# Performance work log

Measured on AMD Instinct MI355X. Metric: run time of the kernel, lower is better.

## Reference

```python
import jax, jax.numpy as jnp
import numpy as np
import math

B, T, C, H, RANK, RD = 8, 512, 2048, 16, 8, 16
HD = C // H  # 128
ADAPTER_SCALE = 1.0 / RANK  # scale / rank with scale=1.0


def setup_inputs() -> dict:
    key = jax.random.key(0)
    ks = jax.random.split(key, 7)
    x = jax.random.normal(ks[0], (B, T, C), dtype=jnp.float32)
    # frozen random linears (weights ~ N(0,1)/sqrt(in_features))
    Wqkv = jax.random.normal(ks[1], (3 * C, C), dtype=jnp.float32) / math.sqrt(C)
    Wout = jax.random.normal(ks[2], (C, C), dtype=jnp.float32) / math.sqrt(C)
    # VeRA frozen random matrices
    A0_qkv = jax.random.normal(ks[3], (RANK, C), dtype=jnp.float32) / math.sqrt(C)
    B0_qkv = jax.random.normal(ks[4], (3 * C, RANK), dtype=jnp.float32) / math.sqrt(RANK)
    A0_out = jax.random.normal(ks[5], (RANK, C), dtype=jnp.float32) / math.sqrt(C)
    B0_out = jax.random.normal(ks[6], (C, RANK), dtype=jnp.float32) / math.sqrt(RANK)
    # learned scaling vectors (init to ones, as in the module)
    d_a_qkv = jnp.ones((RANK,), dtype=jnp.float32)
    d_b_qkv = jnp.ones((RANK,), dtype=jnp.float32)
    d_a_out = jnp.ones((RANK,), dtype=jnp.float32)
    d_b_out = jnp.ones((RANK,), dtype=jnp.float32)
    # partial RoPE caches over first RD dims
    freqs = 1.0 / (10000.0 ** (jnp.arange(0, RD, 2, dtype=jnp.float32) / RD))  # [RD/2]
    ang = jnp.arange(T, dtype=jnp.float32)[:, None] * freqs[None, :]  # [T, RD/2]
    cos = jnp.cos(ang)
    sin = jnp.sin(ang)
    return {"x": x, "Wqkv": Wqkv, "A0_qkv": A0_qkv, "B0_qkv": B0_qkv,
            "d_a_qkv": d_a_qkv, "d_b_qkv": d_b_qkv,
            "Wout": Wout, "A0_out": A0_out, "B0_out": B0_out,
            "d_a_out": d_a_out, "d_b_out": d_b_out,
            "cos": cos, "sin": sin}


def _adapted_linear(x, W, A0, B0, d_a, d_b):
    # frozen(x) + VeRA adapter: diag(d_b) B0 diag(d_a) A0, scaled by 1/rank
    base = x @ W.T
    h = (x @ A0.T) * (d_a * d_b)
    return base + (h @ B0.T) * ADAPTER_SCALE


def _apply_rope(q, cos, sin):
    # q: [B, H, T, HD]; rotate first RD dims, pass-through the rest
    x_rope, x_pass = q[..., :RD], q[..., RD:]
    half = RD // 2
    x1, x2 = x_rope[..., :half], x_rope[..., half:]
    c = cos[None, None]  # [1,1,T,RD/2]
    s = sin[None, None]
    rot = jnp.concatenate([x1 * c - x2 * s, x2 * c + x1 * s], axis=-1)
    return jnp.concatenate([rot, x_pass], axis=-1)


def reference(x, Wqkv, A0_qkv, B0_qkv, d_a_qkv, d_b_qkv,
              Wout, A0_out, B0_out, d_a_out, d_b_out, cos, sin):
    qkv = _adapted_linear(x, Wqkv, A0_qkv, B0_qkv, d_a_qkv, d_b_qkv)  # [B,T,3C]
    qkv = qkv.reshape(B, T, 3, H, HD)
    q = jnp.transpose(qkv[:, :, 0], (0, 2, 1, 3))  # [B,H,T,HD]
    k = jnp.transpose(qkv[:, :, 1], (0, 2, 1, 3))
    v = jnp.transpose(qkv[:, :, 2], (0, 2, 1, 3))
    q = _apply_rope(q, cos, sin)
    k = _apply_rope(k, cos, sin)
    # causal SDPA
    scale = 1.0 / math.sqrt(HD)
    scores = jnp.einsum('bhqd,bhkd->bhqk', q, k) * scale
    mask = jnp.tril(jnp.ones((T, T), dtype=bool))
    scores = jnp.where(mask[None, None], scores, jnp.finfo(scores.dtype).min)
    attn = jax.nn.softmax(scores, axis=-1)
    y = jnp.einsum('bhqk,bhkd->bhqd', attn, v)  # [B,H,T,HD]
    y = jnp.transpose(y, (0, 2, 1, 3)).reshape(B, T, C)
    return _adapted_linear(y, Wout, A0_out, B0_out, d_a_out, d_b_out)
```

## Files before the change

kernel.cpp:

```cpp
#include <hip/hip_runtime.h>

typedef unsigned short ushort_t;
typedef __attribute__((ext_vector_type(8))) short short8;
typedef __attribute__((ext_vector_type(4))) float f32x4;

#define AS1(p) ((const __attribute__((address_space(1))) void*)(p))
#define AS3(p) ((__attribute__((address_space(3))) void*)(p))

__device__ __forceinline__ ushort_t f2bf(float f){
  unsigned u = __float_as_uint(f);
  u += 0x7FFFu + ((u>>16)&1u);
  return (ushort_t)(u>>16);
}
__device__ __forceinline__ float bf2f(ushort_t h){
  return __uint_as_float(((unsigned)h)<<16);
}

__global__ __launch_bounds__(256) void conv_f2b(const float* __restrict__ src,
                                                ushort_t* __restrict__ dst, int n){
  int i = (blockIdx.x*256 + threadIdx.x)*4;
  if (i < n){
    float4 v = *(const float4*)&src[i];
    ushort_t o0=f2bf(v.x), o1=f2bf(v.y), o2=f2bf(v.z), o3=f2bf(v.w);
    ushort4 o; o.x=o0; o.y=o1; o.z=o2; o.w=o3;
    *(ushort4*)&dst[i] = o;
  }
}

template<bool BF16IN>
__global__ __launch_bounds__(256) void lora_h(const void* __restrict__ X,
                                              const float* __restrict__ A0,
                                              const float* __restrict__ da,
                                              const float* __restrict__ db,
                                              float* __restrict__ out, int K){
  int m = blockIdx.x;
  int tid = threadIdx.x, lane = tid & 63, w = tid >> 6;
  float part[8] = {0,0,0,0,0,0,0,0};
  for (int k = tid; k < K; k += 256){
    float xv;
    if (BF16IN) xv = bf2f(((const ushort_t*)X)[(size_t)m*K + k]);
    else        xv = ((const float*)X)[(size_t)m*K + k];
    #pragma unroll
    for (int r=0;r<8;++r) part[r] += xv * A0[r*K + k];
  }
  #pragma unroll
  for (int r=0;r<8;++r)
    for (int d=1;d<64;d<<=1) part[r] += __shfl_xor(part[r], d, 64);
  __shared__ float wsum[4][8];
  if (lane==0){
    #pragma unroll
    for (int r=0;r<8;++r) wsum[w][r] = part[r];
  }
  __syncthreads();
  if (tid < 8){
    float s = wsum[0][tid]+wsum[1][tid]+wsum[2][tid]+wsum[3][tid];
    out[(size_t)m*8 + tid] = s * da[tid]*db[tid];
  }
}

template<int MODE>
__global__ __launch_bounds__(512, 1) void gemm128x256_lora(
    const ushort_t* __restrict__ A, const ushort_t* __restrict__ Bw,
    const float* __restrict__ hmat, const float* __restrict__ B0,
    void* __restrict__ C, int M, int N, int K)
{
  __shared__ __align__(16) char smem[98304];
  const int tid = threadIdx.x, lane = tid & 63, w = tid >> 6;
  const int wm = w >> 2, wn = w & 3;

  const int nbn = N >> 8;
  const int nwg = (M >> 7) * nbn;
  const int q8 = nwg >> 3;
  const int swz = ((int)blockIdx.x & 7)*q8 + ((int)blockIdx.x >> 3);
  const int m0 = (swz / nbn) << 7, n0 = (swz % nbn) << 8;

  const int NTt = K >> 6;

  const int srow8  = tid >> 3;
  const int schunk = (lane & 7) ^ (lane >> 3);

  #define STAGE_AU(u, tt, bb) do { \
    const ushort_t* g_ = A + (size_t)(m0 + (u)*64 + srow8)*K + (tt)*64 + schunk*8; \
    __builtin_amdgcn_global_load_lds(AS1(g_), AS3(smem + (bb)*16384 + (u)*8192 + w*1024), 16, 0, 0); \
  } while(0)
  #define STAGE_BU(u, tt, bb) do { \
    const ushort_t* g_ = Bw + (size_t)(n0 + (u)*64 + srow8)*K + (tt)*64 + schunk*8; \
    __builtin_amdgcn_global_load_lds(AS1(g_), AS3(smem + 32768 + (bb)*32768 + (u)*8192 + w*1024), 16, 0, 0); \
  } while(0)

  #define RDA(bb, q, kk) (*(const short8*)(smem + (bb)*16384 + \
      ((q)*32 + wm*16 + (lane&15))*128 + ((((kk)*4 + (lane>>4)) ^ (lane&7))<<4)))
  #define RDB(bb, rg, kk) (*(const short8*)(smem + 32768 + (bb)*32768 + \
      ((rg)*64 + wn*16 + (lane&15))*128 + ((((kk)*4 + (lane>>4)) ^ (lane&7))<<4)))

  #define MM0(q,rl) do{ \
    acc[q][rl] = __builtin_amdgcn_mfma_f32_16x16x32_bf16(aF[q][0], bF[rl][0], acc[q][rl], 0,0,0); \
    acc[q][rl] = __builtin_amdgcn_mfma_f32_16x16x32_bf16(aF[q][1], bF[rl][1], acc[q][rl], 0,0,0); \
  }while(0)
  #define MM1(q,rl) do{ \
    acc[q][(rl)+2] = __builtin_amdgcn_mfma_f32_16x16x32_bf16(aF[q][0], bF[rl][0], acc[q][(rl)+2], 0,0,0); \
    acc[q][(rl)+2] = __builtin_amdgcn_mfma_f32_16x16x32_bf16(aF[q][1], bF[rl][1], acc[q][(rl)+2], 0,0,0); \
  }while(0)

  #define BARRIER() asm volatile("s_barrier" ::: "memory")

  short8 aF[4][2];
  short8 bF[2][2];
  f32x4 acc[4][4] = {};

  STAGE_AU(0,0,0); STAGE_AU(1,0,0); STAGE_BU(0,0,0); STAGE_BU(1,0,0);
  STAGE_BU(2,0,0); STAGE_BU(3,0,0);
  asm volatile("s_waitcnt vmcnt(2)" ::: "memory");
  BARRIER();

  for (int t = 0; t < NTt-1; ++t){
    const int b = t & 1, nb = b ^ 1;
    #pragma unroll
    for (int q=0;q<4;++q){ aF[q][0]=RDA(b,q,0); aF[q][1]=RDA(b,q,1); }
    #pragma unroll
    for (int rl=0;rl<2;++rl){ bF[rl][0]=RDB(b,rl,0); bF[rl][1]=RDB(b,rl,1); }
    STAGE_AU(0,t+1,nb); STAGE_AU(1,t+1,nb); STAGE_BU(0,t+1,nb); STAGE_BU(1,t+1,nb);
    __builtin_amdgcn_s_setprio(1);
    MM0(0,0); MM0(0,1); MM0(1,0); MM0(1,1);
    MM0(2,0); MM0(2,1); MM0(3,0); MM0(3,1);
    __builtin_amdgcn_s_setprio(0);
    asm volatile("s_waitcnt vmcnt(4)" ::: "memory");
    BARRIER();
    #pragma unroll
    for (int rl=0;rl<2;++rl){ bF[rl][0]=RDB(b,rl+2,0); bF[rl][1]=RDB(b,rl+2,1); }
    STAGE_BU(2,t+1,nb); STAGE_BU(3,t+1,nb);
    __builtin_amdgcn_s_setprio(1);
    MM1(0,0); MM1(0,1); MM1(1,0); MM1(1,1);
    MM1(2,0); MM1(2,1); MM1(3,0); MM1(3,1);
    __builtin_amdgcn_s_setprio(0);
    asm volatile("s_waitcnt lgkmcnt(0)" ::: "memory");
    asm volatile("s_waitcnt vmcnt(2)" ::: "memory");
    BARRIER();
  }

  {
    const int b = (NTt-1) & 1;
    #pragma unroll
    for (int q=0;q<4;++q){ aF[q][0]=RDA(b,q,0); aF[q][1]=RDA(b,q,1); }
    #pragma unroll
    for (int rl=0;rl<2;++rl){ bF[rl][0]=RDB(b,rl,0); bF[rl][1]=RDB(b,rl,1); }
    __builtin_amdgcn_s_setprio(1);
    MM0(0,0); MM0(0,1); MM0(1,0); MM0(1,1);
    MM0(2,0); MM0(2,1); MM0(3,0); MM0(3,1);
    __builtin_amdgcn_s_setprio(0);
    asm volatile("s_waitcnt vmcnt(0)" ::: "memory");
    BARRIER();
    #pragma unroll
    for (int rl=0;rl<2;++rl){ bF[rl][0]=RDB(b,rl+2,0); bF[rl][1]=RDB(b,rl+2,1); }
    MM1(0,0); MM1(0,1); MM1(1,0); MM1(1,1);
    MM1(2,0); MM1(2,1); MM1(3,0); MM1(3,1);
  }

  float b0v[4][8];
  #pragma unroll
  for (int r=0;r<4;++r){
    int col = n0 + r*64 + wn*16 + (lane&15);
    const float4* bp = (const float4*)&B0[(size_t)col*8];
    float4 u0 = bp[0], u1 = bp[1];
    b0v[r][0]=u0.x; b0v[r][1]=u0.y; b0v[r][2]=u0.z; b0v[r][3]=u0.w;
    b0v[r][4]=u1.x; b0v[r][5]=u1.y; b0v[r][6]=u1.z; b0v[r][7]=u1.w;
  }
  #pragma unroll
  for (int q=0;q<4;++q){
    #pragma unroll
    for (int jj=0;jj<4;++jj){
      int row = m0 + q*32 + wm*16 + (lane>>4)*4 + jj;
      const float4* hp = (const float4*)&hmat[(size_t)row*8];
      float4 h0 = hp[0], h1 = hp[1];
      #pragma unroll
      for (int r=0;r<4;++r){
        float lor = h0.x*b0v[r][0]+h0.y*b0v[r][1]+h0.z*b0v[r][2]+h0.w*b0v[r][3]
                  + h1.x*b0v[r][4]+h1.y*b0v[r][5]+h1.z*b0v[r][6]+h1.w*b0v[r][7];
        int col = n0 + r*64 + wn*16 + (lane&15);
        float v = acc[q][r][jj] + 0.125f*lor;
        if (MODE==0) ((ushort_t*)C)[(size_t)row*N + col] = f2bf(v);
        else         ((float*)C)[(size_t)row*N + col]    = v;
      }
    }
  }
  #undef STAGE_AU
  #undef STAGE_BU
  #undef RDA
  #undef RDB
  #undef MM0
  #undef MM1
  #undef BARRIER
}

__global__ __launch_bounds__(256) void rope_kernel(ushort_t* __restrict__ qkv,
                                                   const float* __restrict__ cosb,
                                                   const float* __restrict__ sinb){
  int idx = blockIdx.x*256 + threadIdx.x;
  int d = idx & 7;
  int g = idx >> 3;
  int h_ = g & 15;
  int s  = (g>>4) & 1;
  int t  = (g>>5) & 511;
  int b  = g >> 14;
  size_t base = (size_t)(b*512 + t)*6144 + s*2048 + h_*128;
  float x1 = bf2f(qkv[base+d]), x2 = bf2f(qkv[base+d+8]);
  float c = cosb[t*8+d], sn = sinb[t*8+d];
  qkv[base+d]   = f2bf(x1*c - x2*sn);
  qkv[base+d+8] = f2bf(x2*c + x1*sn);
}

__global__ __launch_bounds__(256) void attn_kernel(const ushort_t* __restrict__ qkv,
                                                   ushort_t* __restrict__ y){
  __shared__ __align__(16) ushort_t Ks[64*128];
  __shared__ __align__(16) ushort_t Vt[128*64];
  __shared__ __align__(16) ushort_t Pl[4][16*64];

  const int qt = blockIdx.x, hh = blockIdx.y, b = blockIdx.z;
  const int tid = threadIdx.x, lane = tid & 63, w = tid >> 6, g = lane >> 4;
  const int qb0 = qt*64;
  const int row_base = b*512;
  const int qoff = hh*128;
  const int koff = 2048 + hh*128;
  const int voff = 4096 + hh*128;
  const float scale = 0.08838834764831845f;

  short8 qf[4];
  {
    int qr = qb0 + w*16 + (lane & 15);
    const ushort_t* qp = qkv + (size_t)(row_base + qr)*6144 + qoff + g*8;
    #pragma unroll
    for (int kc=0;kc<4;++kc) qf[kc] = *(const short8*)(qp + kc*32);
  }

  const int krow = tid >> 4;
  const int kc_  = tid & 15;
  const int kcs  = (kc_ & 8) | ((kc_ ^ (krow & 7)) & 7);
  const int vr   = tid >> 2;
  const int vd0  = (tid & 3) * 32;
  const int vrhi = vr >> 3, vrlo = vr & 7;

  f32x4 o[8] = {};
  float mrow[4] = {-1e30f,-1e30f,-1e30f,-1e30f};
  float lrow[4] = {0,0,0,0};

  for (int t = 0; t <= qt; ++t){
    const int kv0 = t*64;
    __syncthreads();
    {
      const ushort_t* kg = qkv + (size_t)(row_base + kv0 + krow)*6144 + koff + kcs*8;
      #pragma unroll
      for (int i=0;i<4;++i)
        __builtin_amdgcn_global_load_lds(AS1(kg + (size_t)(i*16)*6144),
                                         AS3((char*)Ks + i*4096 + tid*16), 16, 0, 0);
    }
    {
      const ushort_t* vg = qkv + (size_t)(row_base + kv0 + vr)*6144 + voff + vd0;
      short8 vv0 = ((const short8*)vg)[0];
      short8 vv1 = ((const short8*)vg)[1];
      short8 vv2 = ((const short8*)vg)[2];
      short8 vv3 = ((const short8*)vg)[3];
      #pragma unroll
      for (int ii=0;ii<8;++ii){
        int sw = (vrhi ^ ii) << 3;
        Vt[(vd0 + ii     )*64 + sw + vrlo] = (ushort_t)vv0[ii];
        Vt[(vd0 + 8 + ii )*64 + sw + vrlo] = (ushort_t)vv1[ii];
        Vt[(vd0 + 16 + ii)*64 + sw + vrlo] = (ushort_t)vv2[ii];
        Vt[(vd0 + 24 + ii)*64 + sw + vrlo] = (ushort_t)vv3[ii];
      }
    }
    __syncthreads();

    f32x4 s4[4] = {};
    #pragma unroll
    for (int cg=0;cg<4;++cg){
      const int row = cg*16 + (lane&15);
      const int rx = row & 7;
      #pragma unroll
      for (int kc=0;kc<4;++kc){
        const int ch = kc*4 + g;
        const short8 kfv = *(const short8*)&Ks[row*128 + (((ch&8)|((ch^rx)&7))<<3)];
        s4[cg] = __builtin_amdgcn_mfma_f32_16x16x32_bf16(qf[kc], kfv, s4[cg], 0, 0, 0);
      }
    }

    const bool diag = (t == qt);
    float fac[4], p0[4], p1[4], p2[4], p3[4];
    #pragma unroll
    for (int j=0;j<4;++j){
      float a0 = s4[0][j]*scale, a1 = s4[1][j]*scale, a2 = s4[2][j]*scale, a3 = s4[3][j]*scale;
      if (diag){
        int q_abs = qb0 + w*16 + g*4 + j;
        int c0 = kv0 + (lane&15);
        if (c0      > q_abs) a0 = -1e30f;
        if (c0 + 16 > q_abs) a1 = -1e30f;
        if (c0 + 32 > q_abs) a2 = -1e30f;
        if (c0 + 48 > q_abs) a3 = -1e30f;
      }
      float mx = fmaxf(fmaxf(a0,a1), fmaxf(a2,a3));
      #pragma unroll
      for (int d=1; d<16; d<<=1) mx = fmaxf(mx, __shfl_xor(mx, d, 16));
      float mn = fmaxf(mrow[j], mx);
      float f  = __expf(mrow[j] - mn);
      mrow[j] = mn; fac[j] = f;
      p0[j] = __expf(a0 - mn); p1[j] = __expf(a1 - mn);
      p2[j] = __expf(a2 - mn); p3[j] = __expf(a3 - mn);
      float rs = p0[j] + p1[j] + p2[j] + p3[j];
      #pragma unroll
      for (int d=1; d<16; d<<=1) rs += __shfl_xor(rs, d, 16);
      lrow[j] = lrow[j]*f + rs;
    }
    #pragma unroll
    for (int n=0;n<8;++n){
      #pragma unroll
      for (int j=0;j<4;++j) o[n][j] *= fac[j];
    }

    {
      ushort_t* plw = &Pl[w][0];
      #pragma unroll
      for (int j=0;j<4;++j){
        const int prow = g*4 + j;
        const int rx = prow & 7;
        const int cl = (lane&15)>>3, c7 = lane&7;
        plw[prow*64 + (((0*2+cl)^rx)<<3) + c7] = f2bf(p0[j]);
        plw[prow*64 + (((1*2+cl)^rx)<<3) + c7] = f2bf(p1[j]);
        plw[prow*64 + (((2*2+cl)^rx)<<3) + c7] = f2bf(p2[j]);
        plw[prow*64 + (((3*2+cl)^rx)<<3) + c7] = f2bf(p3[j]);
      }
    }
    {
      const ushort_t* plw = &Pl[w][0];
      const int rowP = lane & 15, rxp = rowP & 7;
      const short8 pf0 = *(const short8*)&plw[rowP*64 + (((g  )^rxp)<<3)];
      const short8 pf1 = *(const short8*)&plw[rowP*64 + (((4+g)^rxp)<<3)];
      #pragma unroll
      for (int n=0;n<8;++n){
        const int d = n*16 + (lane&15);
        const int dx = d & 7;
        const short8 vf0 = *(const short8*)&Vt[d*64 + (((g  )^dx)<<3)];
        const short8 vf1 = *(const short8*)&Vt[d*64 + (((4+g)^dx)<<3)];
        o[n] = __builtin_amdgcn_mfma_f32_16x16x32_bf16(pf0, vf0, o[n], 0, 0, 0);
        o[n] = __builtin_amdgcn_mfma_f32_16x16x32_bf16(pf1, vf1, o[n], 0, 0, 0);
      }
    }
  }

  #pragma unroll
  for (int j=0;j<4;++j){
    float inv = 1.0f / lrow[j];
    int qr = qb0 + w*16 + g*4 + j;
    #pragma unroll
    for (int n=0;n<8;++n)
      y[(size_t)(row_base+qr)*2048 + hh*128 + n*16 + (lane&15)] = f2bf(o[n][j]*inv);
  }
}

extern "C" void kernel_launch(void* const* d_in, const int* in_sizes, int n_in,
                              void* d_out, int out_size, void* d_ws, size_t ws_size,
                              hipStream_t stream){
  const float* x       = (const float*)d_in[0];
  const float* Wqkv    = (const float*)d_in[1];
  const float* A0_qkv  = (const float*)d_in[2];
  const float* B0_qkv  = (const float*)d_in[3];
  const float* da_qkv  = (const float*)d_in[4];
  const float* db_qkv  = (const float*)d_in[5];
  const float* Wout    = (const float*)d_in[6];
  const float* A0_out  = (const float*)d_in[7];
  const float* B0_out  = (const float*)d_in[8];
  const float* da_out  = (const float*)d_in[9];
  const float* db_out  = (const float*)d_in[10];
  const float* cosb    = (const float*)d_in[11];
  const float* sinb    = (const float*)d_in[12];
  float* out = (float*)d_out;

  char* ws = (char*)d_ws;
  ushort_t* x_bf    = (ushort_t*)(ws);
  ushort_t* wqkv_bf = (ushort_t*)(ws + 16777216);
  ushort_t* wout_bf = (ushort_t*)(ws + 41943040);
  ushort_t* qkv_bf  = (ushort_t*)(ws + 50331648);
  ushort_t* y_bf    = (ushort_t*)(ws + 100663296);
  float*    h_qkv   = (float*)   (ws + 117440512);
  float*    h_out   = (float*)   (ws + 117571584);

  const int M = 4096;
  const int C = 2048;
  const int N3 = 6144;

  conv_f2b<<<8192, 256, 0, stream>>>(x,    x_bf,    M*C);
  conv_f2b<<<12288,256, 0, stream>>>(Wqkv, wqkv_bf, N3*C);
  conv_f2b<<<4096, 256, 0, stream>>>(Wout, wout_bf, C*C);

  lora_h<false><<<M, 256, 0, stream>>>(x, A0_qkv, da_qkv, db_qkv, h_qkv, C);

  gemm128x256_lora<0><<<(M/128)*(N3/256), 512, 0, stream>>>(x_bf, wqkv_bf, h_qkv, B0_qkv,
                                                            qkv_bf, M, N3, C);

  rope_kernel<<<4096, 256, 0, stream>>>(qkv_bf, cosb, sinb);

  attn_kernel<<<dim3(8, 16, 8), 256, 0, stream>>>(qkv_bf, y_bf);

  lora_h<true><<<M, 256, 0, stream>>>(y_bf, A0_out, da_out, db_out, h_out, C);

  gemm128x256_lora<1><<<(M/128)*(C/256), 512, 0, stream>>>(y_bf, wout_bf, h_out, B0_out,
                                                           out, M, C, C);
}
```

Measured before the change: 272.2 us.

## Use 256x256 tile GEMM for QKV projection and fuse x bf16 conversion into LoRA-h

Adds a new QKV GEMM kernel with a 256x256 output tile per workgroup, double-buffered LDS with interleaved half-tile staging and MFMA phases, and the VeRA adapter epilogue. The larger tile raises operand reuse and halves the number of workgroups. Separately, the fp32-to-bf16 conversion of x is folded into the LoRA h kernel, which already reads x, so the standalone conversion pass goes away. Risks: 96 workgroups on a large-CU device can underfill it, and the per-element ushort writes in the fused kernel are narrow.

```diff
diff --git a/kernel.cpp b/kernel.cpp
--- a/kernel.cpp
+++ b/kernel.cpp
@@ -27,19 +27,18 @@
   }
 }
 
-template<bool BF16IN>
-__global__ __launch_bounds__(256) void lora_h(const void* __restrict__ X,
-                                              const float* __restrict__ A0,
-                                              const float* __restrict__ da,
-                                              const float* __restrict__ db,
-                                              float* __restrict__ out, int K){
+__global__ __launch_bounds__(256) void lora_h_f32(const float* __restrict__ X,
+                                                  ushort_t* __restrict__ Xbf,
+                                                  const float* __restrict__ A0,
+                                                  const float* __restrict__ da,
+                                                  const float* __restrict__ db,
+                                                  float* __restrict__ out, int K){
   int m = blockIdx.x;
   int tid = threadIdx.x, lane = tid & 63, w = tid >> 6;
   float part[8] = {0,0,0,0,0,0,0,0};
   for (int k = tid; k < K; k += 256){
-    float xv;
-    if (BF16IN) xv = bf2f(((const ushort_t*)X)[(size_t)m*K + k]);
-    else        xv = ((const float*)X)[(size_t)m*K + k];
+    float xv = X[(size_t)m*K + k];
+    Xbf[(size_t)m*K + k] = f2bf(xv);
     #pragma unroll
     for (int r=0;r<8;++r) part[r] += xv * A0[r*K + k];
   }
@@ -56,6 +55,203 @@
     float s = wsum[0][tid]+wsum[1][tid]+wsum[2][tid]+wsum[3][tid];
     out[(size_t)m*8 + tid] = s * da[tid]*db[tid];
   }
+}
+
+__global__ __launch_bounds__(256) void lora_h_bf16(const ushort_t* __restrict__ X,
+                                                   const float* __restrict__ A0,
+                                                   const float* __restrict__ da,
+                                                   const float* __restrict__ db,
+                                                   float* __restrict__ out, int K){
+  int m = blockIdx.x;
+  int tid = threadIdx.x, lane = tid & 63, w = tid >> 6;
+  float part[8] = {0,0,0,0,0,0,0,0};
+  for (int k = tid; k < K; k += 256){
+    float xv = bf2f(X[(size_t)m*K + k]);
+    #pragma unroll
+    for (int r=0;r<8;++r) part[r] += xv * A0[r*K + k];
+  }
+  #pragma unroll
+  for (int r=0;r<8;++r)
+    for (int d=1;d<64;d<<=1) part[r] += __shfl_xor(part[r], d, 64);
+  __shared__ float wsum[4][8];
+  if (lane==0){
+    #pragma unroll
+    for (int r=0;r<8;++r) wsum[w][r] = part[r];
+  }
+  __syncthreads();
+  if (tid < 8){
+    float s = wsum[0][tid]+wsum[1][tid]+wsum[2][tid]+wsum[3][tid];
+    out[(size_t)m*8 + tid] = s * da[tid]*db[tid];
+  }
+}
+
+__global__ __launch_bounds__(512, 1) void gemm256_lora(
+    const ushort_t* __restrict__ A, const ushort_t* __restrict__ Bw,
+    const float* __restrict__ hmat, const float* __restrict__ B0,
+    ushort_t* __restrict__ C, int M, int N, int K)
+{
+  __shared__ __align__(16) char smem[131072];
+  const int tid = threadIdx.x, lane = tid & 63, w = tid >> 6;
+  const int wm = w >> 2, wn = w & 3;
+
+  const int nbn = N >> 8;
+  const int nwg = (M >> 8) * nbn;
+  const int q8 = nwg >> 3;
+  const int swz = ((int)blockIdx.x & 7)*q8 + ((int)blockIdx.x >> 3);
+  const int m0 = (swz / nbn) << 8, n0 = (swz % nbn) << 8;
+
+  const int NTt = K >> 6;
+  const int srow   = tid >> 3;
+  const int schunk = (lane & 7) ^ (lane >> 3);
+
+  #define STAGE_A(h, tt, bb) do { \
+    const ushort_t* g_ = A + (size_t)(m0 + (h)*128 + srow)*K + (tt)*64 + schunk*8; \
+    __builtin_amdgcn_global_load_lds(AS1(g_), AS3(smem + (bb)*32768 + (h)*16384 + tid*16), 16, 0, 0); \
+    __builtin_amdgcn_global_load_lds(AS1(g_ + (size_t)64*K), AS3(smem + (bb)*32768 + (h)*16384 + 8192 + tid*16), 16, 0, 0); \
+  } while(0)
+  #define STAGE_B(h, tt, bb) do { \
+    const ushort_t* g_ = Bw + (size_t)(n0 + (h)*128 + srow)*K + (tt)*64 + schunk*8; \
+    __builtin_amdgcn_global_load_lds(AS1(g_), AS3(smem + 65536 + (bb)*32768 + (h)*16384 + tid*16), 16, 0, 0); \
+    __builtin_amdgcn_global_load_lds(AS1(g_ + (size_t)64*K), AS3(smem + 65536 + (bb)*32768 + (h)*16384 + 8192 + tid*16), 16, 0, 0); \
+  } while(0)
+
+  #define RDA(bb, q, kk) (*(const short8*)(smem + (bb)*32768 + ((q)>>2)*16384 + \
+      (((q)&3)*32 + wm*16 + (lane&15))*128 + ((((kk)*4 + (lane>>4)) ^ (lane&7))<<4)))
+  #define RDB(bb, r, kk) (*(const short8*)(smem + 65536 + (bb)*32768 + ((r)>>1)*16384 + \
+      (((r)&1)*64 + wn*16 + (lane&15))*128 + ((((kk)*4 + (lane>>4)) ^ (lane&7))<<4)))
+
+  #define MM(q, ai, r, bi) do{ \
+    acc[q][r] = __builtin_amdgcn_mfma_f32_16x16x32_bf16(aF[ai][0], bF[bi][0], acc[q][r], 0,0,0); \
+    acc[q][r] = __builtin_amdgcn_mfma_f32_16x16x32_bf16(aF[ai][1], bF[bi][1], acc[q][r], 0,0,0); \
+  }while(0)
+
+  #define BARRIER() asm volatile("s_barrier" ::: "memory")
+  #define LGKM0()  do{ asm volatile("s_waitcnt lgkmcnt(0)" ::: "memory"); __builtin_amdgcn_sched_barrier(0); }while(0)
+
+  short8 aF[4][2];
+  short8 bF[2][2];
+  f32x4 acc[8][4] = {};
+
+  STAGE_A(0,0,0); STAGE_B(0,0,0); STAGE_A(1,0,0); STAGE_B(1,0,0);
+  asm volatile("s_waitcnt vmcnt(4)" ::: "memory");
+  BARRIER();
+
+  for (int t = 0; t < NTt-1; ++t){
+    const int b = t & 1, nb = b ^ 1;
+    #pragma unroll
+    for (int q=0;q<4;++q){ aF[q][0]=RDA(b,q,0); aF[q][1]=RDA(b,q,1); }
+    #pragma unroll
+    for (int rl=0;rl<2;++rl){ bF[rl][0]=RDB(b,rl,0); bF[rl][1]=RDB(b,rl,1); }
+    STAGE_A(0, t+1, nb);
+    BARRIER(); LGKM0();
+    __builtin_amdgcn_s_setprio(1);
+    MM(0,0,0,0); MM(0,0,1,1); MM(1,1,0,0); MM(1,1,1,1);
+    MM(2,2,0,0); MM(2,2,1,1); MM(3,3,0,0); MM(3,3,1,1);
+    __builtin_amdgcn_s_setprio(0);
+    asm volatile("s_waitcnt vmcnt(4)" ::: "memory");
+    BARRIER();
+    #pragma unroll
+    for (int q=0;q<4;++q){ aF[q][0]=RDA(b,q+4,0); aF[q][1]=RDA(b,q+4,1); }
+    STAGE_B(0, t+1, nb);
+    BARRIER(); LGKM0();
+    __builtin_amdgcn_s_setprio(1);
+    MM(4,0,0,0); MM(4,0,1,1); MM(5,1,0,0); MM(5,1,1,1);
+    MM(6,2,0,0); MM(6,2,1,1); MM(7,3,0,0); MM(7,3,1,1);
+    __builtin_amdgcn_s_setprio(0);
+    asm volatile("s_waitcnt vmcnt(4)" ::: "memory");
+    BARRIER();
+    #pragma unroll
+    for (int q=0;q<4;++q){ aF[q][0]=RDA(b,q,0); aF[q][1]=RDA(b,q,1); }
+    #pragma unroll
+    for (int rl=0;rl<2;++rl){ bF[rl][0]=RDB(b,rl+2,0); bF[rl][1]=RDB(b,rl+2,1); }
+    STAGE_A(1, t+1, nb);
+    BARRIER(); LGKM0();
+    __builtin_amdgcn_s_setprio(1);
+    MM(0,0,2,0); MM(0,0,3,1); MM(1,1,2,0); MM(1,1,3,1);
+    MM(2,2,2,0); MM(2,2,3,1); MM(3,3,2,0); MM(3,3,3,1);
+    __builtin_amdgcn_s_setprio(0);
+    BARRIER();
+    #pragma unroll
+    for (int q=0;q<4;++q){ aF[q][0]=RDA(b,q+4,0); aF[q][1]=RDA(b,q+4,1); }
+    STAGE_B(1, t+1, nb);
+    BARRIER(); LGKM0();
+    __builtin_amdgcn_s_setprio(1);
+    MM(4,0,2,0); MM(4,0,3,1); MM(5,1,2,0); MM(5,1,3,1);
+    MM(6,2,2,0); MM(6,2,3,1); MM(7,3,2,0); MM(7,3,3,1);
+    __builtin_amdgcn_s_setprio(0);
+    asm volatile("s_waitcnt vmcnt(4)" ::: "memory");
+    BARRIER();
+  }
+
+  {
+    const int b = (NTt-1) & 1;
+    #pragma unroll
+    for (int q=0;q<4;++q){ aF[q][0]=RDA(b,q,0); aF[q][1]=RDA(b,q,1); }
+    #pragma unroll
+    for (int rl=0;rl<2;++rl){ bF[rl][0]=RDB(b,rl,0); bF[rl][1]=RDB(b,rl,1); }
+    BARRIER(); LGKM0();
+    __builtin_amdgcn_s_setprio(1);
+    MM(0,0,0,0); MM(0,0,1,1); MM(1,1,0,0); MM(1,1,1,1);
+    MM(2,2,0,0); MM(2,2,1,1); MM(3,3,0,0); MM(3,3,1,1);
+    __builtin_amdgcn_s_setprio(0);
+    asm volatile("s_waitcnt vmcnt(2)" ::: "memory");
+    BARRIER();
+    #pragma unroll
+    for (int q=0;q<4;++q){ aF[q][0]=RDA(b,q+4,0); aF[q][1]=RDA(b,q+4,1); }
+    BARRIER(); LGKM0();
+    __builtin_amdgcn_s_setprio(1);
+    MM(4,0,0,0); MM(4,0,1,1); MM(5,1,0,0); MM(5,1,1,1);
+    MM(6,2,0,0); MM(6,2,1,1); MM(7,3,0,0); MM(7,3,1,1);
+    __builtin_amdgcn_s_setprio(0);
+    asm volatile("s_waitcnt vmcnt(0)" ::: "memory");
+    BARRIER();
+    #pragma unroll
+    for (int q=0;q<4;++q){ aF[q][0]=RDA(b,q,0); aF[q][1]=RDA(b,q,1); }
+    #pragma unroll
+    for (int rl=0;rl<2;++rl){ bF[rl][0]=RDB(b,rl+2,0); bF[rl][1]=RDB(b,rl+2,1); }
+    LGKM0();
+    MM(0,0,2,0); MM(0,0,3,1); MM(1,1,2,0); MM(1,1,3,1);
+    MM(2,2,2,0); MM(2,2,3,1); MM(3,3,2,0); MM(3,3,3,1);
+    BARRIER();
+    #pragma unroll
+    for (int q=0;q<4;++q){ aF[q][0]=RDA(b,q+4,0); aF[q][1]=RDA(b,q+4,1); }
+    LGKM0();
+    MM(4,0,2,0); MM(4,0,3,1); MM(5,1,2,0); MM(5,1,3,1);
+    MM(6,2,2,0); MM(6,2,3,1); MM(7,3,2,0); MM(7,3,3,1);
+  }
+
+  float b0v[4][8];
+  #pragma unroll
+  for (int r=0;r<4;++r){
+    int col = n0 + r*64 + wn*16 + (lane&15);
+    const float4* bp = (const float4*)&B0[(size_t)col*8];
+    float4 u0 = bp[0], u1 = bp[1];
+    b0v[r][0]=u0.x; b0v[r][1]=u0.y; b0v[r][2]=u0.z; b0v[r][3]=u0.w;
+    b0v[r][4]=u1.x; b0v[r][5]=u1.y; b0v[r][6]=u1.z; b0v[r][7]=u1.w;
+  }
+  #pragma unroll
+  for (int q=0;q<8;++q){
+    #pragma unroll
+    for (int jj=0;jj<4;++jj){
+      int row = m0 + q*32 + wm*16 + (lane>>4)*4 + jj;
+      const float4* hp = (const float4*)&hmat[(size_t)row*8];
+      float4 h0 = hp[0], h1 = hp[1];
+      #pragma unroll
+      for (int r=0;r<4;++r){
+        float lor = h0.x*b0v[r][0]+h0.y*b0v[r][1]+h0.z*b0v[r][2]+h0.w*b0v[r][3]
+                  + h1.x*b0v[r][4]+h1.y*b0v[r][5]+h1.z*b0v[r][6]+h1.w*b0v[r][7];
+        int col = n0 + r*64 + wn*16 + (lane&15);
+        C[(size_t)row*N + col] = f2bf(acc[q][r][jj] + 0.125f*lor);
+      }
+    }
+  }
+  #undef STAGE_A
+  #undef STAGE_B
+  #undef RDA
+  #undef RDB
+  #undef MM
+  #undef BARRIER
+  #undef LGKM0
 }
 
 template<int MODE>
@@ -386,20 +582,19 @@
   const int C = 2048;
   const int N3 = 6144;
 
-  conv_f2b<<<8192, 256, 0, stream>>>(x,    x_bf,    M*C);
   conv_f2b<<<12288,256, 0, stream>>>(Wqkv, wqkv_bf, N3*C);
   conv_f2b<<<4096, 256, 0, stream>>>(Wout, wout_bf, C*C);
 
-  lora_h<false><<<M, 256, 0, stream>>>(x, A0_qkv, da_qkv, db_qkv, h_qkv, C);
-
-  gemm128x256_lora<0><<<(M/128)*(N3/256), 512, 0, stream>>>(x_bf, wqkv_bf, h_qkv, B0_qkv,
-                                                            qkv_bf, M, N3, C);
+  lora_h_f32<<<M, 256, 0, stream>>>(x, x_bf, A0_qkv, da_qkv, db_qkv, h_qkv, C);
+
+  gemm256_lora<<<(M/256)*(N3/256), 512, 0, stream>>>(x_bf, wqkv_bf, h_qkv, B0_qkv,
+                                                     qkv_bf, M, N3, C);
 
   rope_kernel<<<4096, 256, 0, stream>>>(qkv_bf, cosb, sinb);
 
   attn_kernel<<<dim3(8, 16, 8), 256, 0, stream>>>(qkv_bf, y_bf);
 
-  lora_h<true><<<M, 256, 0, stream>>>(y_bf, A0_out, da_out, db_out, h_out, C);
+  lora_h_bf16<<<M, 256, 0, stream>>>(y_bf, A0_out, da_out, db_out, h_out, C);
 
   gemm128x256_lora<1><<<(M/128)*(C/256), 512, 0, stream>>>(y_bf, wout_bf, h_out, B0_out,
                                                            out, M, C, C);
```

Result: no change. 272.5 us (+0.1%).

## Triple-buffer GEMM K-tiles and fuse x bf16 conversion into LoRA down-projection

Applied to the files above, without the earlier changes.

The GEMM main loop moves from a double-buffered, half-tile interleaved schedule to a three-stage LDS ring. Each stage holds a full 128x256x64 tile, loads run two tiles ahead, and each iteration has one barrier. This is meant to hide global-load latency and cut barriers per K-step, at the cost of 144KB of LDS and more B-fragment registers. Separately, the fp32-to-bf16 conversion of x is folded into the lora_h kernel that already reads x, which removes one launch and one full read of x.

```diff
diff --git a/kernel.cpp b/kernel.cpp
--- a/kernel.cpp
+++ b/kernel.cpp
@@ -27,19 +27,46 @@
   }
 }
 
-template<bool BF16IN>
-__global__ __launch_bounds__(256) void lora_h(const void* __restrict__ X,
-                                              const float* __restrict__ A0,
-                                              const float* __restrict__ da,
-                                              const float* __restrict__ db,
-                                              float* __restrict__ out, int K){
+__global__ __launch_bounds__(256) void lora_h_f32(const float* __restrict__ X,
+                                                  ushort_t* __restrict__ Xbf,
+                                                  const float* __restrict__ A0,
+                                                  const float* __restrict__ da,
+                                                  const float* __restrict__ db,
+                                                  float* __restrict__ out, int K){
   int m = blockIdx.x;
   int tid = threadIdx.x, lane = tid & 63, w = tid >> 6;
   float part[8] = {0,0,0,0,0,0,0,0};
   for (int k = tid; k < K; k += 256){
-    float xv;
-    if (BF16IN) xv = bf2f(((const ushort_t*)X)[(size_t)m*K + k]);
-    else        xv = ((const float*)X)[(size_t)m*K + k];
+    float xv = X[(size_t)m*K + k];
+    Xbf[(size_t)m*K + k] = f2bf(xv);
+    #pragma unroll
+    for (int r=0;r<8;++r) part[r] += xv * A0[r*K + k];
+  }
+  #pragma unroll
+  for (int r=0;r<8;++r)
+    for (int d=1;d<64;d<<=1) part[r] += __shfl_xor(part[r], d, 64);
+  __shared__ float wsum[4][8];
+  if (lane==0){
+    #pragma unroll
+    for (int r=0;r<8;++r) wsum[w][r] = part[r];
+  }
+  __syncthreads();
+  if (tid < 8){
+    float s = wsum[0][tid]+wsum[1][tid]+wsum[2][tid]+wsum[3][tid];
+    out[(size_t)m*8 + tid] = s * da[tid]*db[tid];
+  }
+}
+
+__global__ __launch_bounds__(256) void lora_h_bf16(const ushort_t* __restrict__ X,
+                                                   const float* __restrict__ A0,
+                                                   const float* __restrict__ da,
+                                                   const float* __restrict__ db,
+                                                   float* __restrict__ out, int K){
+  int m = blockIdx.x;
+  int tid = threadIdx.x, lane = tid & 63, w = tid >> 6;
+  float part[8] = {0,0,0,0,0,0,0,0};
+  for (int k = tid; k < K; k += 256){
+    float xv = bf2f(X[(size_t)m*K + k]);
     #pragma unroll
     for (int r=0;r<8;++r) part[r] += xv * A0[r*K + k];
   }
@@ -64,7 +91,7 @@
     const float* __restrict__ hmat, const float* __restrict__ B0,
     void* __restrict__ C, int M, int N, int K)
 {
-  __shared__ __align__(16) char smem[98304];
+  __shared__ __align__(16) char smem[147456];
   const int tid = threadIdx.x, lane = tid & 63, w = tid >> 6;
   const int wm = w >> 2, wn = w & 3;
 
@@ -81,79 +108,82 @@
 
   #define STAGE_AU(u, tt, bb) do { \
     const ushort_t* g_ = A + (size_t)(m0 + (u)*64 + srow8)*K + (tt)*64 + schunk*8; \
-    __builtin_amdgcn_global_load_lds(AS1(g_), AS3(smem + (bb)*16384 + (u)*8192 + w*1024), 16, 0, 0); \
+    __builtin_amdgcn_global_load_lds(AS1(g_), AS3(smem + (bb)*49152 + (u)*8192 + w*1024), 16, 0, 0); \
   } while(0)
   #define STAGE_BU(u, tt, bb) do { \
     const ushort_t* g_ = Bw + (size_t)(n0 + (u)*64 + srow8)*K + (tt)*64 + schunk*8; \
-    __builtin_amdgcn_global_load_lds(AS1(g_), AS3(smem + 32768 + (bb)*32768 + (u)*8192 + w*1024), 16, 0, 0); \
+    __builtin_amdgcn_global_load_lds(AS1(g_), AS3(smem + (bb)*49152 + 16384 + (u)*8192 + w*1024), 16, 0, 0); \
   } while(0)
-
-  #define RDA(bb, q, kk) (*(const short8*)(smem + (bb)*16384 + \
+  #define STAGE_TILE(tt, bb) do { \
+    STAGE_AU(0,tt,bb); STAGE_AU(1,tt,bb); \
+    STAGE_BU(0,tt,bb); STAGE_BU(1,tt,bb); STAGE_BU(2,tt,bb); STAGE_BU(3,tt,bb); \
+  } while(0)
+
+  #define RDA(bb, q, kk) (*(const short8*)(smem + (bb)*49152 + \
       ((q)*32 + wm*16 + (lane&15))*128 + ((((kk)*4 + (lane>>4)) ^ (lane&7))<<4)))
-  #define RDB(bb, rg, kk) (*(const short8*)(smem + 32768 + (bb)*32768 + \
+  #define RDB(bb, rg, kk) (*(const short8*)(smem + (bb)*49152 + 16384 + \
       ((rg)*64 + wn*16 + (lane&15))*128 + ((((kk)*4 + (lane>>4)) ^ (lane&7))<<4)))
 
-  #define MM0(q,rl) do{ \
-    acc[q][rl] = __builtin_amdgcn_mfma_f32_16x16x32_bf16(aF[q][0], bF[rl][0], acc[q][rl], 0,0,0); \
-    acc[q][rl] = __builtin_amdgcn_mfma_f32_16x16x32_bf16(aF[q][1], bF[rl][1], acc[q][rl], 0,0,0); \
+  #define MM(q,r) do{ \
+    acc[q][r] = __builtin_amdgcn_mfma_f32_16x16x32_bf16(aF[q][0], bF[r][0], acc[q][r], 0,0,0); \
+    acc[q][r] = __builtin_amdgcn_mfma_f32_16x16x32_bf16(aF[q][1], bF[r][1], acc[q][r], 0,0,0); \
   }while(0)
-  #define MM1(q,rl) do{ \
-    acc[q][(rl)+2] = __builtin_amdgcn_mfma_f32_16x16x32_bf16(aF[q][0], bF[rl][0], acc[q][(rl)+2], 0,0,0); \
-    acc[q][(rl)+2] = __builtin_amdgcn_mfma_f32_16x16x32_bf16(aF[q][1], bF[rl][1], acc[q][(rl)+2], 0,0,0); \
-  }while(0)
 
   #define BARRIER() asm volatile("s_barrier" ::: "memory")
 
   short8 aF[4][2];
-  short8 bF[2][2];
+  short8 bF[4][2];
   f32x4 acc[4][4] = {};
 
-  STAGE_AU(0,0,0); STAGE_AU(1,0,0); STAGE_BU(0,0,0); STAGE_BU(1,0,0);
-  STAGE_BU(2,0,0); STAGE_BU(3,0,0);
-  asm volatile("s_waitcnt vmcnt(2)" ::: "memory");
+  STAGE_TILE(0, 0);
+  STAGE_TILE(1, 1);
+  asm volatile("s_waitcnt vmcnt(6)" ::: "memory");
   BARRIER();
 
-  for (int t = 0; t < NTt-1; ++t){
-    const int b = t & 1, nb = b ^ 1;
-    #pragma unroll
-    for (int q=0;q<4;++q){ aF[q][0]=RDA(b,q,0); aF[q][1]=RDA(b,q,1); }
-    #pragma unroll
-    for (int rl=0;rl<2;++rl){ bF[rl][0]=RDB(b,rl,0); bF[rl][1]=RDB(b,rl,1); }
-    STAGE_AU(0,t+1,nb); STAGE_AU(1,t+1,nb); STAGE_BU(0,t+1,nb); STAGE_BU(1,t+1,nb);
+  int cb = 0;
+  for (int t = 0; t < NTt-2; ++t){
+    const int sb = (cb >= 1) ? cb - 1 : 2;
+    STAGE_TILE(t+2, sb);
+    #pragma unroll
+    for (int q=0;q<4;++q){ aF[q][0]=RDA(cb,q,0); aF[q][1]=RDA(cb,q,1); }
+    #pragma unroll
+    for (int r=0;r<4;++r){ bF[r][0]=RDB(cb,r,0); bF[r][1]=RDB(cb,r,1); }
     __builtin_amdgcn_s_setprio(1);
-    MM0(0,0); MM0(0,1); MM0(1,0); MM0(1,1);
-    MM0(2,0); MM0(2,1); MM0(3,0); MM0(3,1);
-    __builtin_amdgcn_s_setprio(0);
-    asm volatile("s_waitcnt vmcnt(4)" ::: "memory");
-    BARRIER();
-    #pragma unroll
-    for (int rl=0;rl<2;++rl){ bF[rl][0]=RDB(b,rl+2,0); bF[rl][1]=RDB(b,rl+2,1); }
-    STAGE_BU(2,t+1,nb); STAGE_BU(3,t+1,nb);
-    __builtin_amdgcn_s_setprio(1);
-    MM1(0,0); MM1(0,1); MM1(1,0); MM1(1,1);
-    MM1(2,0); MM1(2,1); MM1(3,0); MM1(3,1);
+    MM(0,0); MM(0,1); MM(0,2); MM(0,3);
+    MM(1,0); MM(1,1); MM(1,2); MM(1,3);
+    MM(2,0); MM(2,1); MM(2,2); MM(2,3);
+    MM(3,0); MM(3,1); MM(3,2); MM(3,3);
     __builtin_amdgcn_s_setprio(0);
     asm volatile("s_waitcnt lgkmcnt(0)" ::: "memory");
-    asm volatile("s_waitcnt vmcnt(2)" ::: "memory");
+    asm volatile("s_waitcnt vmcnt(6)" ::: "memory");
     BARRIER();
+    cb = (cb == 2) ? 0 : cb + 1;
   }
 
   {
-    const int b = (NTt-1) & 1;
-    #pragma unroll
-    for (int q=0;q<4;++q){ aF[q][0]=RDA(b,q,0); aF[q][1]=RDA(b,q,1); }
-    #pragma unroll
-    for (int rl=0;rl<2;++rl){ bF[rl][0]=RDB(b,rl,0); bF[rl][1]=RDB(b,rl,1); }
+    #pragma unroll
+    for (int q=0;q<4;++q){ aF[q][0]=RDA(cb,q,0); aF[q][1]=RDA(cb,q,1); }
+    #pragma unroll
+    for (int r=0;r<4;++r){ bF[r][0]=RDB(cb,r,0); bF[r][1]=RDB(cb,r,1); }
     __builtin_amdgcn_s_setprio(1);
-    MM0(0,0); MM0(0,1); MM0(1,0); MM0(1,1);
-    MM0(2,0); MM0(2,1); MM0(3,0); MM0(3,1);
+    MM(0,0); MM(0,1); MM(0,2); MM(0,3);
+    MM(1,0); MM(1,1); MM(1,2); MM(1,3);
+    MM(2,0); MM(2,1); MM(2,2); MM(2,3);
+    MM(3,0); MM(3,1); MM(3,2); MM(3,3);
     __builtin_amdgcn_s_setprio(0);
     asm volatile("s_waitcnt vmcnt(0)" ::: "memory");
     BARRIER();
-    #pragma unroll
-    for (int rl=0;rl<2;++rl){ bF[rl][0]=RDB(b,rl+2,0); bF[rl][1]=RDB(b,rl+2,1); }
-    MM1(0,0); MM1(0,1); MM1(1,0); MM1(1,1);
-    MM1(2,0); MM1(2,1); MM1(3,0); MM1(3,1);
+    cb = (cb == 2) ? 0 : cb + 1;
+  }
+  {
+    #pragma unroll
+    for (int q=0;q<4;++q){ aF[q][0]=RDA(cb,q,0); aF[q][1]=RDA(cb,q,1); }
+    #pragma unroll
+    for (int r=0;r<4;++r){ bF[r][0]=RDB(cb,r,0); bF[r][1]=RDB(cb,r,1); }
+    MM(0,0); MM(0,1); MM(0,2); MM(0,3);
+    MM(1,0); MM(1,1); MM(1,2); MM(1,3);
+    MM(2,0); MM(2,1); MM(2,2); MM(2,3);
+    MM(3,0); MM(3,1); MM(3,2); MM(3,3);
   }
 
   float b0v[4][8];
@@ -185,10 +215,10 @@
   }
   #undef STAGE_AU
   #undef STAGE_BU
+  #undef STAGE_TILE
   #undef RDA
   #undef RDB
-  #undef MM0
-  #undef MM1
+  #undef MM
   #undef BARRIER
 }
 
@@ -386,11 +416,10 @@
   const int C = 2048;
   const int N3 = 6144;
 
-  conv_f2b<<<8192, 256, 0, stream>>>(x,    x_bf,    M*C);
   conv_f2b<<<12288,256, 0, stream>>>(Wqkv, wqkv_bf, N3*C);
   conv_f2b<<<4096, 256, 0, stream>>>(Wout, wout_bf, C*C);
 
-  lora_h<false><<<M, 256, 0, stream>>>(x, A0_qkv, da_qkv, db_qkv, h_qkv, C);
+  lora_h_f32<<<M, 256, 0, stream>>>(x, x_bf, A0_qkv, da_qkv, db_qkv, h_qkv, C);
 
   gemm128x256_lora<0><<<(M/128)*(N3/256), 512, 0, stream>>>(x_bf, wqkv_bf, h_qkv, B0_qkv,
                                                             qkv_bf, M, N3, C);
@@ -399,7 +428,7 @@
 
   attn_kernel<<<dim3(8, 16, 8), 256, 0, stream>>>(qkv_bf, y_bf);
 
-  lora_h<true><<<M, 256, 0, stream>>>(y_bf, A0_out, da_out, db_out, h_out, C);
+  lora_h_bf16<<<M, 256, 0, stream>>>(y_bf, A0_out, da_out, db_out, h_out, C);
 
   gemm128x256_lora<1><<<(M/128)*(C/256), 512, 0, stream>>>(y_bf, wout_bf, h_out, B0_out,
                                                            out, M, C, C);
```

Result: no change. 275.9 us (+1.4%).
